# Optimization experiments

Measured on AMD Instinct MI355X. Metric: run time of the kernel, lower is better.

The kernel has to match this reference:

```python
import jax, jax.numpy as jnp
import numpy as np

N_ATOMS = 100000
N_EDGES = 6400000
R_MAX = 6.0
KE = 14.3996


def inverse_softplus(x):
    return np.log(np.expm1(x))


def setup_inputs() -> dict:
    key = jax.random.key(0)
    k_r, k_z, k_i, k_j = jax.random.split(key, 4)
    R = jax.random.normal(k_r, (N_ATOMS, 3), dtype=jnp.float32) * 10.0
    Z = jax.random.randint(k_z, (N_ATOMS,), 1, 50, dtype=jnp.int32)
    idx_i = jax.random.randint(k_i, (N_EDGES,), 0, N_ATOMS, dtype=jnp.int32)
    idx_j = jax.random.randint(k_j, (N_EDGES,), 0, N_ATOMS, dtype=jnp.int32)
    idx = jnp.stack([idx_i, idx_j], axis=0)  # [2, E]
    box = jnp.zeros((3,), dtype=jnp.float32)
    offsets = jnp.zeros((N_EDGES, 3), dtype=jnp.float32)
    # learned params stored in inverse-softplus space, as in setup()
    a_exp = jnp.full((1,), inverse_softplus(0.23), dtype=jnp.float32)
    a_num = jnp.full((1,), inverse_softplus(0.4685), dtype=jnp.float32)
    coefficients = jnp.asarray(
        inverse_softplus(np.array([0.18175, 0.50986, 0.28022, 0.02817])[:, None]),
        dtype=jnp.float32)
    exponents = jnp.asarray(
        inverse_softplus(np.array([3.1998, 0.94229, 0.4029, 0.20162])[:, None]),
        dtype=jnp.float32)
    rep_scale = jnp.full((1,), inverse_softplus(1.0 / KE), dtype=jnp.float32)
    return {"R": R, "Z": Z, "idx": idx, "box": box, "offsets": offsets,
            "a_exp": a_exp, "a_num": a_num, "coefficients": coefficients,
            "exponents": exponents, "rep_scale": rep_scale}


def reference(R, Z, idx, box, offsets, a_exp, a_num, coefficients, exponents, rep_scale):
    idx_i, idx_j = idx[0], idx[1]
    Zf = Z.astype(R.dtype)
    Z_i = Zf[idx_i]  # [E]
    Z_j = Zf[idx_j]  # [E]
    # free-space displacement: R[idx_j] - R[idx_i]  (box/offsets unused)
    dr_vec = R[idx_j] - R[idx_i]                     # [E, 3]
    dr = jnp.sqrt(jnp.sum(dr_vec * dr_vec, axis=-1))  # [E]
    dr = jnp.clip(dr, 0.02, R_MAX)
    cos_cutoff = 0.5 * (jnp.cos(np.pi * dr / R_MAX) + 1.0)
    sp = jax.nn.softplus
    ae = sp(a_exp)           # (1,)
    an = sp(a_num)           # (1,)
    c = sp(coefficients)     # (4, 1)
    e = sp(exponents)        # (4, 1)
    rs = sp(rep_scale)       # (1,)
    a_divisor = Z_i ** ae + Z_j ** ae              # [E]
    dist = dr * a_divisor / an                     # [E]
    f = jnp.sum(c * jnp.exp(-e * dist), axis=0)    # (4,E) -> [E]
    E_ij = Z_i * Z_j / dr * f * cos_cutoff         # [E]
    mask = (idx_i != idx_j).astype(E_ij.dtype)     # padded self-edges masked
    E = 0.5 * rs * KE * jnp.sum(E_ij * mask)       # (1,)
    return jnp.sum(E)                              # scalar
```

## Files before the change

kernel.cpp:

```cpp
#include <hip/hip_runtime.h>

#ifndef KE_CONST
#define KE_CONST 14.3996f
#endif

constexpr float R_MAX_C = 6.0f;
constexpr float LOG2E = 1.4426950408889634f;
constexpr float LN2 = 0.6931471805599453f;

typedef int vint4 __attribute__((ext_vector_type(4)));

__device__ __forceinline__ float fast_exp2(float x) { return __builtin_amdgcn_exp2f(x); }
__device__ __forceinline__ float fast_log2(float x) { return __builtin_amdgcn_logf(x); }
__device__ __forceinline__ float fast_exp(float x) { return __builtin_amdgcn_exp2f(x * LOG2E); }
__device__ __forceinline__ float cos_rev(float rev) { return __builtin_amdgcn_cosf(rev); }
__device__ __forceinline__ float fast_sqrt(float x) { return __builtin_amdgcn_sqrtf(x); }
__device__ __forceinline__ float fast_rcp(float x) { return __builtin_amdgcn_rcpf(x); }

__device__ __forceinline__ float softplus_f(float x) {
    return LN2 * fast_log2(1.0f + fast_exp(x));
}

__global__ void pack_atoms_kernel(const float* __restrict__ R,
                                  const int* __restrict__ Z,
                                  float4* __restrict__ atoms, int n,
                                  float* __restrict__ out) {
    int t = blockIdx.x * blockDim.x + threadIdx.x;
    if (t == 0) out[0] = 0.0f;
    if (t < n) {
        atoms[t] = make_float4(R[3 * t + 0], R[3 * t + 1], R[3 * t + 2],
                               (float)Z[t]);
    }
}

struct EdgeParams {
    float inv_an, c0, c1, c2, c3, e0, e1, e2, e3;
};

__device__ __forceinline__ float edge_term(const float4& ai, const float4& aj,
                                           const EdgeParams& p,
                                           const float* __restrict__ zpow_lut) {
    float dx = aj.x - ai.x, dy = aj.y - ai.y, dz = aj.z - ai.z;
    float dr = fast_sqrt(dx * dx + dy * dy + dz * dz);
    dr = fminf(fmaxf(dr, 0.02f), R_MAX_C);
    float cc = 0.5f * (cos_rev(dr * (1.0f / 12.0f)) + 1.0f);
    float zpi = zpow_lut[(int)ai.w];
    float zpj = zpow_lut[(int)aj.w];
    float dist = dr * (zpi + zpj) * p.inv_an;
    float f = p.c0 * fast_exp(-p.e0 * dist) + p.c1 * fast_exp(-p.e1 * dist) +
              p.c2 * fast_exp(-p.e2 * dist) + p.c3 * fast_exp(-p.e3 * dist);
    return ai.w * aj.w * fast_rcp(dr) * f * cc;
}

__global__ __launch_bounds__(256, 4) void edge_energy_kernel(
    const int* __restrict__ idx,
    const float4* __restrict__ atoms,
    const float* __restrict__ a_exp, const float* __restrict__ a_num,
    const float* __restrict__ coefficients, const float* __restrict__ exponents,
    const float* __restrict__ rep_scale,
    float* __restrict__ out, int nEdges) {
    __shared__ float zpow_lut[64];
    __shared__ float smem[4];

    const float ae = softplus_f(a_exp[0]);
    if (threadIdx.x < 64) {
        float z = (float)(threadIdx.x == 0 ? 1 : threadIdx.x);
        zpow_lut[threadIdx.x] = fast_exp2(ae * fast_log2(z));
    }

    EdgeParams p;
    p.inv_an = fast_rcp(softplus_f(a_num[0]));
    p.c0 = softplus_f(coefficients[0]);
    p.c1 = softplus_f(coefficients[1]);
    p.c2 = softplus_f(coefficients[2]);
    p.c3 = softplus_f(coefficients[3]);
    p.e0 = softplus_f(exponents[0]);
    p.e1 = softplus_f(exponents[1]);
    p.e2 = softplus_f(exponents[2]);
    p.e3 = softplus_f(exponents[3]);
    const float scale = 0.5f * softplus_f(rep_scale[0]) * KE_CONST;
    __syncthreads();

    const long long tid = (long long)blockIdx.x * blockDim.x + threadIdx.x;
    const long long base = tid * 8;

    float acc = 0.0f;
    if (base + 8 <= (long long)nEdges) {
        const vint4* __restrict__ i4 = (const vint4*)(idx) + (base >> 2);
        const vint4* __restrict__ j4 = (const vint4*)(idx + nEdges) + (base >> 2);
        vint4 ia = i4[0];
        vint4 ib = i4[1];
        vint4 ja = j4[0];
        vint4 jb = j4[1];
        int ii[8] = {ia.x, ia.y, ia.z, ia.w, ib.x, ib.y, ib.z, ib.w};
        int jj[8] = {ja.x, ja.y, ja.z, ja.w, jb.x, jb.y, jb.z, jb.w};
        float4 A[8], B[8];
#pragma unroll
        for (int u = 0; u < 8; ++u) {
            A[u] = atoms[ii[u]];
            B[u] = atoms[jj[u]];
        }
        __builtin_amdgcn_sched_barrier(0);
#pragma unroll
        for (int u = 0; u < 8; ++u) {
            float e = edge_term(A[u], B[u], p, zpow_lut);
            acc += (ii[u] != jj[u]) ? e : 0.0f;
        }
    } else if (base < (long long)nEdges) {
        for (long long t = base; t < (long long)nEdges; ++t) {
            int i = idx[t], j = idx[nEdges + t];
            float4 ai = atoms[i];
            float4 aj = atoms[j];
            float e = edge_term(ai, aj, p, zpow_lut);
            acc += (i != j) ? e : 0.0f;
        }
    }

#pragma unroll
    for (int off = 32; off > 0; off >>= 1) acc += __shfl_down(acc, off, 64);
    const int lane = threadIdx.x & 63;
    const int wave = threadIdx.x >> 6;
    if (lane == 0) smem[wave] = acc;
    __syncthreads();
    if (threadIdx.x == 0) {
        float s = (smem[0] + smem[1]) + (smem[2] + smem[3]);
        atomicAdd(out, s * scale);
    }
}

extern "C" void kernel_launch(void* const* d_in, const int* in_sizes, int n_in,
                              void* d_out, int out_size, void* d_ws, size_t ws_size,
                              hipStream_t stream) {
    const float* R = (const float*)d_in[0];
    const int* Z = (const int*)d_in[1];
    const int* idx = (const int*)d_in[2];
    const float* a_exp = (const float*)d_in[5];
    const float* a_num = (const float*)d_in[6];
    const float* coefficients = (const float*)d_in[7];
    const float* exponents = (const float*)d_in[8];
    const float* rep_scale = (const float*)d_in[9];

    const int nAtoms = in_sizes[0] / 3;
    const int nEdges = in_sizes[2] / 2;
    float* out = (float*)d_out;

    float4* atoms = (float4*)d_ws;
    pack_atoms_kernel<<<(nAtoms + 255) / 256, 256, 0, stream>>>(R, Z, atoms,
                                                                nAtoms, out);
    const int edges_per_block = 256 * 8;
    const int blocks = (nEdges + edges_per_block - 1) / edges_per_block;
    edge_energy_kernel<<<blocks, 256, 0, stream>>>(
        idx, atoms, a_exp, a_num, coefficients, exponents, rep_scale, out,
        nEdges);
}
```

Measured before the change: 198.6 us.

## Skip beyond-cutoff edges, move params to SGPRs, raise occupancy bound

Skips the exp, cos and rcp work for edges whose squared distance is at least the cutoff squared, where the cosine cutoff term is exactly zero. Self-edge masking becomes a per-edge bitmask. Scalar parameters are computed after the gather loads are issued and forced into scalar registers through readfirstlane, and launch bounds rise from 4 to 6 waves to allow more occupancy. Because the random atom positions put most edges past the cutoff, this should save ALU work, but the kernel is likely limited by the gather memory traffic and the branch can diverge within a wave.

```diff
diff --git a/kernel.cpp b/kernel.cpp
--- a/kernel.cpp
+++ b/kernel.cpp
@@ -4,7 +4,6 @@
 #define KE_CONST 14.3996f
 #endif
 
-constexpr float R_MAX_C = 6.0f;
 constexpr float LOG2E = 1.4426950408889634f;
 constexpr float LN2 = 0.6931471805599453f;
 
@@ -21,6 +20,10 @@
     return LN2 * fast_log2(1.0f + fast_exp(x));
 }
 
+__device__ __forceinline__ float to_sgpr(float x) {
+    return __uint_as_float((unsigned)__builtin_amdgcn_readfirstlane((int)__float_as_uint(x)));
+}
+
 __global__ void pack_atoms_kernel(const float* __restrict__ R,
                                   const int* __restrict__ Z,
                                   float4* __restrict__ atoms, int n,
@@ -33,26 +36,7 @@
     }
 }
 
-struct EdgeParams {
-    float inv_an, c0, c1, c2, c3, e0, e1, e2, e3;
-};
-
-__device__ __forceinline__ float edge_term(const float4& ai, const float4& aj,
-                                           const EdgeParams& p,
-                                           const float* __restrict__ zpow_lut) {
-    float dx = aj.x - ai.x, dy = aj.y - ai.y, dz = aj.z - ai.z;
-    float dr = fast_sqrt(dx * dx + dy * dy + dz * dz);
-    dr = fminf(fmaxf(dr, 0.02f), R_MAX_C);
-    float cc = 0.5f * (cos_rev(dr * (1.0f / 12.0f)) + 1.0f);
-    float zpi = zpow_lut[(int)ai.w];
-    float zpj = zpow_lut[(int)aj.w];
-    float dist = dr * (zpi + zpj) * p.inv_an;
-    float f = p.c0 * fast_exp(-p.e0 * dist) + p.c1 * fast_exp(-p.e1 * dist) +
-              p.c2 * fast_exp(-p.e2 * dist) + p.c3 * fast_exp(-p.e3 * dist);
-    return ai.w * aj.w * fast_rcp(dr) * f * cc;
-}
-
-__global__ __launch_bounds__(256, 4) void edge_energy_kernel(
+__global__ __launch_bounds__(256, 6) void edge_energy_kernel(
     const int* __restrict__ idx,
     const float4* __restrict__ atoms,
     const float* __restrict__ a_exp, const float* __restrict__ a_num,
@@ -62,30 +46,24 @@
     __shared__ float zpow_lut[64];
     __shared__ float smem[4];
 
-    const float ae = softplus_f(a_exp[0]);
-    if (threadIdx.x < 64) {
-        float z = (float)(threadIdx.x == 0 ? 1 : threadIdx.x);
-        zpow_lut[threadIdx.x] = fast_exp2(ae * fast_log2(z));
+    {
+        const float ae = softplus_f(a_exp[0]);
+        if (threadIdx.x < 64) {
+            float z = (float)(threadIdx.x == 0 ? 1 : threadIdx.x);
+            zpow_lut[threadIdx.x] = fast_exp2(ae * fast_log2(z));
+        }
     }
-
-    EdgeParams p;
-    p.inv_an = fast_rcp(softplus_f(a_num[0]));
-    p.c0 = softplus_f(coefficients[0]);
-    p.c1 = softplus_f(coefficients[1]);
-    p.c2 = softplus_f(coefficients[2]);
-    p.c3 = softplus_f(coefficients[3]);
-    p.e0 = softplus_f(exponents[0]);
-    p.e1 = softplus_f(exponents[1]);
-    p.e2 = softplus_f(exponents[2]);
-    p.e3 = softplus_f(exponents[3]);
-    const float scale = 0.5f * softplus_f(rep_scale[0]) * KE_CONST;
     __syncthreads();
 
     const long long tid = (long long)blockIdx.x * blockDim.x + threadIdx.x;
     const long long base = tid * 8;
+    const bool full = (base + 8 <= (long long)nEdges);
 
+    float4 A[8], B[8];
+    unsigned live = 0;
     float acc = 0.0f;
-    if (base + 8 <= (long long)nEdges) {
+
+    if (full) {
         const vint4* __restrict__ i4 = (const vint4*)(idx) + (base >> 2);
         const vint4* __restrict__ j4 = (const vint4*)(idx + nEdges) + (base >> 2);
         vint4 ia = i4[0];
@@ -94,25 +72,64 @@
         vint4 jb = j4[1];
         int ii[8] = {ia.x, ia.y, ia.z, ia.w, ib.x, ib.y, ib.z, ib.w};
         int jj[8] = {ja.x, ja.y, ja.z, ja.w, jb.x, jb.y, jb.z, jb.w};
-        float4 A[8], B[8];
+#pragma unroll
+        for (int u = 0; u < 8; ++u) live |= (ii[u] != jj[u] ? 1u : 0u) << u;
 #pragma unroll
         for (int u = 0; u < 8; ++u) {
             A[u] = atoms[ii[u]];
             B[u] = atoms[jj[u]];
         }
         __builtin_amdgcn_sched_barrier(0);
+    }
+
+    const float inv_an = to_sgpr(fast_rcp(softplus_f(a_num[0])));
+    const float c0 = to_sgpr(softplus_f(coefficients[0]));
+    const float c1 = to_sgpr(softplus_f(coefficients[1]));
+    const float c2 = to_sgpr(softplus_f(coefficients[2]));
+    const float c3 = to_sgpr(softplus_f(coefficients[3]));
+    const float e0 = to_sgpr(softplus_f(exponents[0]));
+    const float e1 = to_sgpr(softplus_f(exponents[1]));
+    const float e2 = to_sgpr(softplus_f(exponents[2]));
+    const float e3 = to_sgpr(softplus_f(exponents[3]));
+    const float scale = to_sgpr(0.5f * softplus_f(rep_scale[0]) * KE_CONST);
+
+    if (full) {
 #pragma unroll
         for (int u = 0; u < 8; ++u) {
-            float e = edge_term(A[u], B[u], p, zpow_lut);
-            acc += (ii[u] != jj[u]) ? e : 0.0f;
+            float dx = B[u].x - A[u].x;
+            float dy = B[u].y - A[u].y;
+            float dz = B[u].z - A[u].z;
+            float dr2 = dx * dx + dy * dy + dz * dz;
+            if (dr2 < 36.0f && ((live >> u) & 1u)) {
+                float dr = fmaxf(fast_sqrt(dr2), 0.02f);
+                float cc = 0.5f * (cos_rev(dr * (1.0f / 12.0f)) + 1.0f);
+                float zpi = zpow_lut[(int)A[u].w];
+                float zpj = zpow_lut[(int)B[u].w];
+                float dist = dr * (zpi + zpj) * inv_an;
+                float f = c0 * fast_exp(-e0 * dist) + c1 * fast_exp(-e1 * dist) +
+                          c2 * fast_exp(-e2 * dist) + c3 * fast_exp(-e3 * dist);
+                acc += A[u].w * B[u].w * fast_rcp(dr) * f * cc;
+            }
         }
     } else if (base < (long long)nEdges) {
         for (long long t = base; t < (long long)nEdges; ++t) {
             int i = idx[t], j = idx[nEdges + t];
             float4 ai = atoms[i];
             float4 aj = atoms[j];
-            float e = edge_term(ai, aj, p, zpow_lut);
-            acc += (i != j) ? e : 0.0f;
+            float dx = aj.x - ai.x;
+            float dy = aj.y - ai.y;
+            float dz = aj.z - ai.z;
+            float dr2 = dx * dx + dy * dy + dz * dz;
+            if (dr2 < 36.0f && i != j) {
+                float dr = fmaxf(fast_sqrt(dr2), 0.02f);
+                float cc = 0.5f * (cos_rev(dr * (1.0f / 12.0f)) + 1.0f);
+                float zpi = zpow_lut[(int)ai.w];
+                float zpj = zpow_lut[(int)aj.w];
+                float dist = dr * (zpi + zpj) * inv_an;
+                float f = c0 * fast_exp(-e0 * dist) + c1 * fast_exp(-e1 * dist) +
+                          c2 * fast_exp(-e2 * dist) + c3 * fast_exp(-e3 * dist);
+                acc += ai.w * aj.w * fast_rcp(dr) * f * cc;
+            }
         }
     }
 
```

Result: slower. 252.3 us (+27.0%).
